# Kernel optimization log

Hardware: AMD Instinct MI355X
Metric: run time of the kernel (lower is better)

The kernel has to match this reference:

```python
import jax, jax.numpy as jnp
import numpy as np
import math

B, S, D = 4, 1024, 1024
H, DK = 16, 64
NUM_BUCKETS, MAX_DIST = 32, 128


def _relative_position_bucket(relative_position, num_buckets=NUM_BUCKETS, max_distance=MAX_DIST):
    # bidirectional bucketing (T5 encoder style)
    num_buckets = num_buckets // 2
    buckets = (relative_position > 0).astype(jnp.int32) * num_buckets
    rp = jnp.abs(relative_position)
    max_exact = num_buckets // 2
    is_small = rp < max_exact
    # clamp to >=1 to avoid log(0); masked out by is_small anyway
    rp_large = max_exact + (
        jnp.log(jnp.maximum(rp, 1).astype(jnp.float32) / max_exact)
        / math.log(max_distance / max_exact)
        * (num_buckets - max_exact)
    ).astype(jnp.int32)
    rp_large = jnp.minimum(rp_large, num_buckets - 1)
    return buckets + jnp.where(is_small, rp, rp_large)


def compute_bias(rel_bias_table, q_len, k_len):
    ctx = jnp.arange(q_len)[:, None]
    mem = jnp.arange(k_len)[None, :]
    buckets = _relative_position_bucket(mem - ctx)  # [q,k]
    values = rel_bias_table[buckets]  # [q,k,H]
    return jnp.transpose(values, (2, 0, 1))  # [H,q,k]


def setup_inputs() -> dict:
    key = jax.random.key(0)
    ks = jax.random.split(key, 6)
    return {
        "hidden_states": jax.random.normal(ks[0], (B, S, D), dtype=jnp.float32),
        "Wq": jax.random.normal(ks[1], (D, H * DK), dtype=jnp.float32) * 0.02,
        "Wk": jax.random.normal(ks[2], (D, H * DK), dtype=jnp.float32) * 0.02,
        "Wv": jax.random.normal(ks[3], (D, H * DK), dtype=jnp.float32) * 0.02,
        "Wo": jax.random.normal(ks[4], (H * DK, D), dtype=jnp.float32) * 0.02,
        "rel_bias_table": jax.random.normal(ks[5], (NUM_BUCKETS, H), dtype=jnp.float32),
    }


def reference(hidden_states, Wq, Wk, Wv, Wo, rel_bias_table):
    b, s, _ = hidden_states.shape
    # projections (no bias), split heads -> [b,h,s,dk]
    def heads(x):
        return jnp.transpose(x.reshape(b, s, H, DK), (0, 2, 1, 3))
    q = heads(hidden_states @ Wq)
    k = heads(hidden_states @ Wk)
    v = heads(hidden_states @ Wv)
    # NOTE: T5 attention is UNSCALED (no 1/sqrt(dk))
    scores = jnp.einsum("bhqd,bhkd->bhqk", q, k)
    bias = compute_bias(rel_bias_table, s, s)[None]  # [1,H,s,s]
    scores = scores + bias
    attn = jax.nn.softmax(scores.astype(jnp.float32), axis=-1).astype(scores.dtype)
    out = jnp.einsum("bhqk,bhkd->bhqd", attn, v)
    out = jnp.transpose(out, (0, 2, 1, 3)).reshape(b, s, H * DK)
    return out @ Wo
```

## Files before the change

### kernel.cpp

```cpp
#include <hip/hip_runtime.h>
#include <hip/hip_bf16.h>

typedef __attribute__((ext_vector_type(8))) short short8;
typedef __attribute__((ext_vector_type(4))) float f32x4;
typedef __attribute__((ext_vector_type(4))) unsigned u32x4;
typedef unsigned short u16;

#define AS1 __attribute__((address_space(1)))
#define AS3 __attribute__((address_space(3)))

#define LOG2E 1.44269504088896f
#define FOLD_M 46.166241308446828f
#define EXP2(x) __builtin_amdgcn_exp2f(x)
#define WAITV(n) asm volatile("s_waitcnt vmcnt(" #n ")" ::: "memory")
#define BAR() __builtin_amdgcn_s_barrier()

__device__ __forceinline__ u16 f2bf(float f) {
    unsigned u = __builtin_bit_cast(unsigned, f);
    u += 0x7FFFu + ((u >> 16) & 1u);
    return (u16)(u >> 16);
}

__device__ __forceinline__ unsigned pk2(float a, float b) {
    unsigned ua = __builtin_bit_cast(unsigned, a) + 0x8000u;
    unsigned ub = __builtin_bit_cast(unsigned, b) + 0x8000u;
    return __builtin_amdgcn_perm(ub, ua, 0x07060302);
}

__global__ __launch_bounds__(256) void k_prep(const float* __restrict__ hidden,
                                              const float* __restrict__ Wq, const float* __restrict__ Wk,
                                              const float* __restrict__ Wv, const float* __restrict__ Wo,
                                              const float* __restrict__ tbl,
                                              u16* __restrict__ hidb,
                                              u16* __restrict__ wt, u16* __restrict__ wot,
                                              float* __restrict__ bias2) {
    int z = blockIdx.z;
    if (z >= 5) {
        int i = ((z - 5) * 1024 + blockIdx.y * 32 + blockIdx.x) * 256 + threadIdx.x;
        float4 v = ((const float4*)hidden)[i];
        ushort4 o;
        o.x = f2bf(v.x); o.y = f2bf(v.y); o.z = f2bf(v.z); o.w = f2bf(v.w);
        ((ushort4*)hidb)[i] = o;
        return;
    }
    if (z == 4) {
        int idx = (blockIdx.y * 32 + blockIdx.x) * 256 + threadIdx.x;
        if (idx < 16 * 2048) {
            int r = idx & 2047, h = idx >> 11;
            int rel = r - 1023;
            int bucket = rel > 0 ? 16 : 0;
            int rp = rel < 0 ? -rel : rel;
            if (rp < 8) bucket += rp;
            else {
                int lb = 8 + (int)(log2f((float)rp * 0.125f) * 2.0f);
                bucket += (lb < 15 ? lb : 15);
            }
            bias2[idx] = tbl[bucket * 16 + h] * LOG2E - FOLD_M;
        }
        return;
    }
    const float* in = z == 0 ? Wq : z == 1 ? Wk : z == 2 ? Wv : Wo;
    u16* out = (z == 3) ? wot : wt + (size_t)z * 1024 * 1024;
    __shared__ float tile[32][33];
    int tx = threadIdx.x & 31, ty = threadIdx.x >> 5;
    int bx = blockIdx.x << 5, by = blockIdx.y << 5;
    #pragma unroll
    for (int j = 0; j < 32; j += 8)
        tile[ty + j][tx] = in[(size_t)(by + ty + j) * 1024 + bx + tx];
    __syncthreads();
    #pragma unroll
    for (int j = 0; j < 32; j += 8)
        out[(size_t)(bx + ty + j) * 1024 + by + tx] = f2bf(tile[tx][ty + j]);
}

__global__ __launch_bounds__(512, 2) void k_qkv(const u16* __restrict__ A, const u16* __restrict__ Bt,
                                                u16* __restrict__ oq, u16* __restrict__ ok,
                                                u16* __restrict__ ov) {
    __shared__ __align__(16) u16 As[2][256 * 64];
    __shared__ __align__(16) u16 Bs[2][192 * 64];
    int t = threadIdx.x, lane = t & 63, wave = t >> 6;
    int g = lane >> 4, ln = lane & 15;
    int wr = wave >> 2, wc = wave & 3;

    int bid = blockIdx.x;
    int xcd = bid & 7, wgl = bid >> 3;
    int mt = ((xcd & 3) << 2) + (wgl >> 3);
    int nt = ((xcd >> 2) << 3) + (wgl & 7);
    int m0 = mt << 8, n0 = nt * 192;

    f32x4 acc[8][3];
    #pragma unroll
    for (int i = 0; i < 8; i++)
        #pragma unroll
        for (int j = 0; j < 3; j++) acc[i][j] = (f32x4){0.f, 0.f, 0.f, 0.f};

    #define QSTG(kt_, buf_)                                                                      \
        {                                                                                        \
            _Pragma("unroll")                                                                    \
            for (int u = 0; u < 4; u++) {                                                        \
                int L = t * 16 + u * 8192;                                                       \
                int row = L >> 7, gI = (L >> 4) & 7, gp = gI ^ (row & 7);                        \
                __builtin_amdgcn_global_load_lds(                                                \
                    (const AS1 void*)(A + (size_t)(m0 + row) * 1024 + (kt_) * 64 + gp * 8),      \
                    (AS3 void*)&As[buf_][L >> 1], 16, 0, 0);                                     \
            }                                                                                    \
            _Pragma("unroll")                                                                    \
            for (int u = 0; u < 3; u++) {                                                        \
                int L = t * 16 + u * 8192;                                                       \
                int row = L >> 7, gI = (L >> 4) & 7, gp = gI ^ (row & 7);                        \
                __builtin_amdgcn_global_load_lds(                                                \
                    (const AS1 void*)(Bt + (size_t)(n0 + row) * 1024 + (kt_) * 64 + gp * 8),     \
                    (AS3 void*)&Bs[buf_][L >> 1], 16, 0, 0);                                     \
            }                                                                                    \
        }

    QSTG(0, 0);

    #pragma unroll 2
    for (int kt = 0; kt < 16; kt++) {
        const int c = kt & 1;
        if (kt < 15) {
            QSTG(kt + 1, c ^ 1);
            WAITV(7);
        } else {
            WAITV(0);
        }
        BAR();

        #pragma unroll
        for (int ks = 0; ks < 2; ks++) {
            short8 af[8], bfr[3];
            int cb = ((ks << 2) + g) << 4;
            #pragma unroll
            for (int mf = 0; mf < 8; mf++) {
                int row = (wr << 7) + (mf << 4) + ln;
                af[mf] = *(const short8*)((const char*)&As[c][0] + row * 128 + (cb ^ ((row & 7) << 4)));
            }
            #pragma unroll
            for (int nf = 0; nf < 3; nf++) {
                int row = wc * 48 + (nf << 4) + ln;
                bfr[nf] = *(const short8*)((const char*)&Bs[c][0] + row * 128 + (cb ^ ((row & 7) << 4)));
            }
            #pragma unroll
            for (int mf = 0; mf < 8; mf++)
                #pragma unroll
                for (int nf = 0; nf < 3; nf++)
                    acc[mf][nf] = __builtin_amdgcn_mfma_f32_16x16x32_bf16(af[mf], bfr[nf], acc[mf][nf], 0, 0, 0);
        }
        BAR();
    }
    #undef QSTG

    #pragma unroll
    for (int mf = 0; mf < 8; mf++)
        #pragma unroll
        for (int nf = 0; nf < 3; nf++) {
            int mb = m0 + (wr << 7) + (mf << 4) + (g << 2);
            int n = n0 + wc * 48 + (nf << 4) + ln;
            int j = n >> 10, col = n & 1023;
            int h = col >> 6, dk = col & 63;
            int b = mb >> 10, s = mb & 1023;
            if (j == 2) {
                ushort4 pk;
                pk.x = f2bf(acc[mf][nf][0]); pk.y = f2bf(acc[mf][nf][1]);
                pk.z = f2bf(acc[mf][nf][2]); pk.w = f2bf(acc[mf][nf][3]);
                *(ushort4*)(ov + ((size_t)(((b << 4) + h) * 64 + dk)) * 1024 + s) = pk;
            } else {
                u16* dst = (j == 0) ? oq : ok;
                #pragma unroll
                for (int r = 0; r < 4; r++)
                    dst[((size_t)(((b << 4) + h) * 1024 + s + r)) * 64 + dk] = f2bf(acc[mf][nf][r]);
            }
        }
}

__global__ __launch_bounds__(256) void k_gemm_out(const u16* __restrict__ A, const u16* __restrict__ Bt,
                                                  float* __restrict__ outf) {
    const int K = 1024, N = 1024;
    __shared__ __align__(16) u16 As[2][8192];
    __shared__ __align__(16) u16 Bs[2][8192];
    int t = threadIdx.x, lane = t & 63, wave = t >> 6;
    int bid = blockIdx.y * 8 + blockIdx.x;
    int sbid = (bid & 7) * 32 + (bid >> 3);
    int m0 = (sbid >> 3) << 7, n0 = (sbid & 7) << 7;
    int wm = (wave >> 1) << 6, wn = (wave & 1) << 6;
    int g = lane >> 4, ln = lane & 15;
    f32x4 acc[4][4];
    #pragma unroll
    for (int i = 0; i < 4; i++)
        #pragma unroll
        for (int j = 0; j < 4; j++) acc[i][j] = (f32x4){0.f, 0.f, 0.f, 0.f};

    int schunk = ((lane & 3) ^ ((lane >> 3) & 3)) << 3;
    const u16* gA = A + (size_t)(m0 + wave * 16 + (lane >> 2)) * K + schunk;
    const u16* gB = Bt + (size_t)(n0 + wave * 16 + (lane >> 2)) * K + schunk;
    int ldsOff = wave * 512;

    #define GSTAGE(k0_, buf_)                                                                          \
        {                                                                                              \
            __builtin_amdgcn_global_load_lds((const AS1 void*)(gA + (k0_)),                            \
                                             (AS3 void*)&As[buf_][ldsOff], 16, 0, 0);                  \
            __builtin_amdgcn_global_load_lds((const AS1 void*)(gA + 64 * K + (k0_)),                   \
                                             (AS3 void*)&As[buf_][ldsOff + 2048], 16, 0, 0);           \
            __builtin_amdgcn_global_load_lds((const AS1 void*)(gB + (k0_)),                            \
                                             (AS3 void*)&Bs[buf_][ldsOff], 16, 0, 0);                  \
            __builtin_amdgcn_global_load_lds((const AS1 void*)(gB + 64 * K + (k0_)),                   \
                                             (AS3 void*)&Bs[buf_][ldsOff + 2048], 16, 0, 0);           \
        }

    GSTAGE(0, 0);

    int rchunk = (g ^ ((ln >> 1) & 3)) << 3;

    #pragma unroll 2
    for (int kb = 0; kb < 32; kb++) {
        const int cur = kb & 1;
        if (kb < 31) {
            GSTAGE((kb + 1) * 32, cur ^ 1);
            WAITV(4);
        } else {
            WAITV(0);
        }
        BAR();

        short8 af[4], bfr[4];
        #pragma unroll
        for (int fm = 0; fm < 4; fm++)
            af[fm] = *(const short8*)&As[cur][(wm + (fm << 4) + ln) * 32 + rchunk];
        #pragma unroll
        for (int fn = 0; fn < 4; fn++)
            bfr[fn] = *(const short8*)&Bs[cur][(wn + (fn << 4) + ln) * 32 + rchunk];
        #pragma unroll
        for (int fm = 0; fm < 4; fm++)
            #pragma unroll
            for (int fn = 0; fn < 4; fn++)
                acc[fm][fn] = __builtin_amdgcn_mfma_f32_16x16x32_bf16(af[fm], bfr[fn], acc[fm][fn], 0, 0, 0);

        BAR();
    }

    #pragma unroll
    for (int fm = 0; fm < 4; fm++)
        #pragma unroll
        for (int fn = 0; fn < 4; fn++) {
            int mb = m0 + wm + (fm << 4) + (g << 2);
            int n = n0 + wn + (fn << 4) + ln;
            #pragma unroll
            for (int r = 0; r < 4; r++)
                outf[(size_t)(mb + r) * N + n] = acc[fm][fn][r];
        }
    #undef GSTAGE
}

__global__ __launch_bounds__(256, 2) void k_attn(const u16* __restrict__ Qg, const u16* __restrict__ Kg,
                                                 const u16* __restrict__ Vtg, const float* __restrict__ bias2,
                                                 u16* __restrict__ attn_out) {
    __shared__ __align__(16) u16 Ks[2][64 * 64];
    __shared__ __align__(16) u16 Vts[2][64 * 64];
    __shared__ __align__(16) float blds4[4][1160];

    int t = threadIdx.x, lane = t & 63, w = t >> 6;
    int bid = blockIdx.x;
    int sid = (bid & 7) * 64 + (bid >> 3);
    int qb = sid & 7, h = (sid >> 3) & 15, b = sid >> 7;
    int q0 = qb << 7;
    const u16* Qh = Qg + ((size_t)(((b << 4) + h) * 1024 + q0)) * 64;
    const u16* Kh = Kg + (size_t)(((b << 4) + h)) * 1024 * 64;
    const u16* Vth = Vtg + (size_t)(((b << 4) + h)) * 64 * 1024;
    const float* bh = bias2 + (h << 11);

    int g = lane >> 4, ln = lane & 15;
    int lnk = (ln & 3) | ((ln & 4) << 1) | ((ln & 8) >> 1);
    int kbq = ((g & 1) << 3) | ((g >> 1) << 2);

    short8 qf[2][2];
    #pragma unroll
    for (int fm = 0; fm < 2; fm++)
        #pragma unroll
        for (int kh = 0; kh < 2; kh++)
            qf[fm][kh] = *(const short8*)(Qh + (size_t)(w * 32 + fm * 16 + ln) * 64 + kh * 32 + g * 8);

    int w0 = 896 - q0;
    for (int i = t; i < 1152; i += 256) {
        float v = bh[w0 + i];
        #pragma unroll
        for (int a2 = 0; a2 < 4; a2++) { int x = i - a2; if (x >= 0) blds4[a2][x] = v; }
    }
    float b_hi = bh[1023 + 256];
    float b_lo = bh[1023 - 256];
    int aRep = (3 - ln) & 3;
    const float* repB = &blds4[aRep][0];

    #define STAGE(kb_, buf_)                                                                     \
        {                                                                                        \
            _Pragma("unroll")                                                                    \
            for (int r2 = 0; r2 < 2; r2++) {                                                     \
                int L = t * 16 + r2 * 4096;                                                      \
                int row = L >> 7, gI = (L >> 4) & 7, gp = gI ^ (row & 7);                        \
                __builtin_amdgcn_global_load_lds(                                                \
                    (const AS1 void*)(Kh + (size_t)((kb_) * 64 + row) * 64 + gp * 8),            \
                    (AS3 void*)&Ks[buf_][L >> 1], 16, 0, 0);                                     \
                __builtin_amdgcn_global_load_lds(                                                \
                    (const AS1 void*)(Vth + (size_t)row * 1024 + (kb_) * 64 + gp * 8),           \
                    (AS3 void*)&Vts[buf_][L >> 1], 16, 0, 0);                                    \
            }                                                                                    \
        }

    STAGE(0, 0);
    asm volatile("s_waitcnt lgkmcnt(0)" ::: "memory");
    __syncthreads();

    float psum[2] = {0.f, 0.f};
    f32x4 o[2][4];
    #pragma unroll
    for (int fm = 0; fm < 2; fm++)
        #pragma unroll
        for (int dn = 0; dn < 4; dn++) o[fm][dn] = (f32x4){0.f, 0.f, 0.f, 0.f};

    #pragma unroll 2
    for (int kb = 0; kb < 16; kb++) {
        const int cur = kb & 1;
        if (kb < 15) {
            STAGE(kb + 1, cur ^ 1);
            WAITV(4);
        } else {
            WAITV(0);
        }
        BAR();

        f32x4 s[2][4];
        __builtin_amdgcn_s_setprio(1);
        #pragma unroll
        for (int fn = 0; fn < 4; fn++) {
            int row = (fn << 4) + lnk;
            short8 kf0 = *(const short8*)((const char*)Ks[cur] + row * 128 + (((g << 4) + 0)  ^ ((row & 7) << 4)));
            short8 kf1 = *(const short8*)((const char*)Ks[cur] + row * 128 + (((g << 4) + 64) ^ ((row & 7) << 4)));
            #pragma unroll
            for (int fm = 0; fm < 2; fm++) {
                f32x4 a = (f32x4){0.f, 0.f, 0.f, 0.f};
                a = __builtin_amdgcn_mfma_f32_16x16x32_bf16(kf0, qf[fm][0], a, 0, 0, 0);
                a = __builtin_amdgcn_mfma_f32_16x16x32_bf16(kf1, qf[fm][1], a, 0, 0, 0);
                s[fm][fn] = a;
            }
        }
        __builtin_amdgcn_s_setprio(0);

        int d0 = 64 * kb - q0 - 32 * w;
        int ibase = 64 * kb - 32 * w + 127 + kbq - ln;
        bool fast = (d0 >= 122) || (d0 <= -154);
        float bu = d0 > 0 ? b_hi : b_lo;
        unsigned Px[2][4], Py[2][4];
        #pragma unroll
        for (int fm = 0; fm < 2; fm++)
            #pragma unroll
            for (int fn = 0; fn < 4; fn++) {
                f32x4 sv = s[fm][fn];
                float b0, b1, b2v, b3;
                if (fast) { b0 = b1 = b2v = b3 = bu; }
                else {
                    float4 bb = *(const float4*)(repB + (ibase + 16 * fn - 16 * fm - aRep));
                    b0 = bb.x; b1 = bb.y; b2v = bb.z; b3 = bb.w;
                }
                float p0 = EXP2(fmaf(sv[0], LOG2E, b0));
                float p1 = EXP2(fmaf(sv[1], LOG2E, b1));
                float p2 = EXP2(fmaf(sv[2], LOG2E, b2v));
                float p3 = EXP2(fmaf(sv[3], LOG2E, b3));
                psum[fm] += (p0 + p1) + (p2 + p3);
                Px[fm][fn] = pk2(p0, p1);
                Py[fm][fn] = pk2(p2, p3);
            }

        short8 pa[2][2];
        #pragma unroll
        for (int fm = 0; fm < 2; fm++)
            #pragma unroll
            for (int ks = 0; ks < 2; ks++) {
                unsigned w0r = Px[fm][2 * ks], w2r = Px[fm][2 * ks + 1];
                unsigned w1r = Py[fm][2 * ks], w3r = Py[fm][2 * ks + 1];
                asm volatile("s_nop 1\n\tv_permlane32_swap_b32 %0, %1" : "+v"(w0r), "+v"(w2r));
                asm volatile("s_nop 1\n\tv_permlane32_swap_b32 %0, %1" : "+v"(w1r), "+v"(w3r));
                u32x4 tv; tv[0] = w0r; tv[1] = w1r; tv[2] = w2r; tv[3] = w3r;
                pa[fm][ks] = __builtin_bit_cast(short8, tv);
            }

        __builtin_amdgcn_s_setprio(1);
        #pragma unroll
        for (int dn = 0; dn < 4; dn++) {
            int vrow = (dn << 4) + ln;
            short8 vb0 = *(const short8*)((const char*)Vts[cur] + vrow * 128 + (((g << 4) + 0)  ^ ((vrow & 7) << 4)));
            short8 vb1 = *(const short8*)((const char*)Vts[cur] + vrow * 128 + (((g << 4) + 64) ^ ((vrow & 7) << 4)));
            #pragma unroll
            for (int fm = 0; fm < 2; fm++) {
                f32x4 a = o[fm][dn];
                a = __builtin_amdgcn_mfma_f32_16x16x32_bf16(pa[fm][0], vb0, a, 0, 0, 0);
                a = __builtin_amdgcn_mfma_f32_16x16x32_bf16(pa[fm][1], vb1, a, 0, 0, 0);
                o[fm][dn] = a;
            }
        }
        __builtin_amdgcn_s_setprio(0);

        BAR();
    }

    float linv[2][4];
    #pragma unroll
    for (int fm = 0; fm < 2; fm++) {
        float v = psum[fm];
        v += __shfl_xor(v, 16);
        v += __shfl_xor(v, 32);
        float inv = 1.0f / v;
        #pragma unroll
        for (int r = 0; r < 4; r++)
            linv[fm][r] = __shfl(inv, 4 * g + r);
    }
    #pragma unroll
    for (int fm = 0; fm < 2; fm++)
        #pragma unroll
        for (int dn = 0; dn < 4; dn++)
            #pragma unroll
            for (int r = 0; r < 4; r++) {
                int srow = q0 + 32 * w + 16 * fm + (g << 2) + r;
                int col = (h << 6) + (dn << 4) + ln;
                attn_out[((size_t)((b << 10) + srow) << 10) + col] = f2bf(o[fm][dn][r] * linv[fm][r]);
            }
}

extern "C" void kernel_launch(void* const* d_in, const int* in_sizes, int n_in,
                              void* d_out, int out_size, void* d_ws, size_t ws_size,
                              hipStream_t stream) {
    const float* hidden = (const float*)d_in[0];
    const float* Wq = (const float*)d_in[1];
    const float* Wk = (const float*)d_in[2];
    const float* Wv = (const float*)d_in[3];
    const float* Wo = (const float*)d_in[4];
    const float* tbl = (const float*)d_in[5];

    u16* hidb = (u16*)d_ws;
    u16* wt   = hidb + 4096 * 1024;
    u16* wot  = wt + 3072 * 1024;
    u16* Qb   = wot + 1024 * 1024;
    u16* Kb   = Qb + 4 * 16 * 1024 * 64;
    u16* Vb   = Kb + 4 * 16 * 1024 * 64;
    u16* attn = Vb + 4 * 16 * 1024 * 64;
    float* bias = (float*)(attn + 4096 * 1024);

    k_prep<<<dim3(32, 32, 9), 256, 0, stream>>>(hidden, Wq, Wk, Wv, Wo, tbl, hidb, wt, wot, bias);
    k_qkv<<<256, 512, 0, stream>>>(hidb, wt, Qb, Kb, Vb);
    k_attn<<<512, 256, 0, stream>>>(Qb, Kb, Vb, bias, attn);
    k_gemm_out<<<dim3(8, 32), 256, 0, stream>>>(attn, wot, (float*)d_out);
}
```

Before: 93.99 us.

## Load K/V fragments directly from global memory, dropping LDS staging and barriers

The attention kernel stops staging K and V tiles into double-buffered shared memory with global_load_lds and barriers. Each wave now loads its MFMA fragments for K and V straight from global memory, relying on L1/L2 caching for reuse across the four waves. The launch bound rises to 3 blocks per CU since LDS use drops. Each wave now reads K and V redundantly, and there is no explicit prefetch, so load latency may be exposed.

```diff
diff --git a/kernel.cpp b/kernel.cpp
--- a/kernel.cpp
+++ b/kernel.cpp
@@ -252,11 +252,9 @@
     #undef GSTAGE
 }
 
-__global__ __launch_bounds__(256, 2) void k_attn(const u16* __restrict__ Qg, const u16* __restrict__ Kg,
+__global__ __launch_bounds__(256, 3) void k_attn(const u16* __restrict__ Qg, const u16* __restrict__ Kg,
                                                  const u16* __restrict__ Vtg, const float* __restrict__ bias2,
                                                  u16* __restrict__ attn_out) {
-    __shared__ __align__(16) u16 Ks[2][64 * 64];
-    __shared__ __align__(16) u16 Vts[2][64 * 64];
     __shared__ __align__(16) float blds4[4][1160];
 
     int t = threadIdx.x, lane = t & 63, w = t >> 6;
@@ -291,24 +289,10 @@
     int aRep = (3 - ln) & 3;
     const float* repB = &blds4[aRep][0];
 
-    #define STAGE(kb_, buf_)                                                                     \
-        {                                                                                        \
-            _Pragma("unroll")                                                                    \
-            for (int r2 = 0; r2 < 2; r2++) {                                                     \
-                int L = t * 16 + r2 * 4096;                                                      \
-                int row = L >> 7, gI = (L >> 4) & 7, gp = gI ^ (row & 7);                        \
-                __builtin_amdgcn_global_load_lds(                                                \
-                    (const AS1 void*)(Kh + (size_t)((kb_) * 64 + row) * 64 + gp * 8),            \
-                    (AS3 void*)&Ks[buf_][L >> 1], 16, 0, 0);                                     \
-                __builtin_amdgcn_global_load_lds(                                                \
-                    (const AS1 void*)(Vth + (size_t)row * 1024 + (kb_) * 64 + gp * 8),           \
-                    (AS3 void*)&Vts[buf_][L >> 1], 16, 0, 0);                                    \
-            }                                                                                    \
-        }
-
-    STAGE(0, 0);
-    asm volatile("s_waitcnt lgkmcnt(0)" ::: "memory");
     __syncthreads();
+
+    const u16* Kf = Kh + (size_t)lnk * 64 + g * 8;
+    const u16* Vf = Vth + (size_t)ln * 1024 + g * 8;
 
     float psum[2] = {0.f, 0.f};
     f32x4 o[2][4];
@@ -319,22 +303,13 @@
 
     #pragma unroll 2
     for (int kb = 0; kb < 16; kb++) {
-        const int cur = kb & 1;
-        if (kb < 15) {
-            STAGE(kb + 1, cur ^ 1);
-            WAITV(4);
-        } else {
-            WAITV(0);
-        }
-        BAR();
-
         f32x4 s[2][4];
         __builtin_amdgcn_s_setprio(1);
         #pragma unroll
         for (int fn = 0; fn < 4; fn++) {
-            int row = (fn << 4) + lnk;
-            short8 kf0 = *(const short8*)((const char*)Ks[cur] + row * 128 + (((g << 4) + 0)  ^ ((row & 7) << 4)));
-            short8 kf1 = *(const short8*)((const char*)Ks[cur] + row * 128 + (((g << 4) + 64) ^ ((row & 7) << 4)));
+            const u16* kr = Kf + (size_t)kb * 4096 + fn * 1024;
+            short8 kf0 = *(const short8*)(kr);
+            short8 kf1 = *(const short8*)(kr + 32);
             #pragma unroll
             for (int fm = 0; fm < 2; fm++) {
                 f32x4 a = (f32x4){0.f, 0.f, 0.f, 0.f};
@@ -344,6 +319,14 @@
             }
         }
         __builtin_amdgcn_s_setprio(0);
+
+        short8 vb[4][2];
+        #pragma unroll
+        for (int dn = 0; dn < 4; dn++) {
+            const u16* vr = Vf + dn * 16384 + kb * 64;
+            vb[dn][0] = *(const short8*)(vr);
+            vb[dn][1] = *(const short8*)(vr + 32);
+        }
 
         int d0 = 64 * kb - q0 - 32 * w;
         int ibase = 64 * kb - 32 * w + 127 + kbq - ln;
@@ -385,21 +368,15 @@
 
         __builtin_amdgcn_s_setprio(1);
         #pragma unroll
-        for (int dn = 0; dn < 4; dn++) {
-            int vrow = (dn << 4) + ln;
-            short8 vb0 = *(const short8*)((const char*)Vts[cur] + vrow * 128 + (((g << 4) + 0)  ^ ((vrow & 7) << 4)));
-            short8 vb1 = *(const short8*)((const char*)Vts[cur] + vrow * 128 + (((g << 4) + 64) ^ ((vrow & 7) << 4)));
+        for (int dn = 0; dn < 4; dn++)
             #pragma unroll
             for (int fm = 0; fm < 2; fm++) {
                 f32x4 a = o[fm][dn];
-                a = __builtin_amdgcn_mfma_f32_16x16x32_bf16(pa[fm][0], vb0, a, 0, 0, 0);
-                a = __builtin_amdgcn_mfma_f32_16x16x32_bf16(pa[fm][1], vb1, a, 0, 0, 0);
+                a = __builtin_amdgcn_mfma_f32_16x16x32_bf16(pa[fm][0], vb[dn][0], a, 0, 0, 0);
+                a = __builtin_amdgcn_mfma_f32_16x16x32_bf16(pa[fm][1], vb[dn][1], a, 0, 0, 0);
                 o[fm][dn] = a;
             }
-        }
         __builtin_amdgcn_s_setprio(0);
-
-        BAR();
     }
 
     float linv[2][4];
```

After: 164.8 us. +75.4%, slower.

## Retile QKV GEMM to 128x128 tiles with 256-thread blocks and BK=32

Applied to the files above, without the earlier changes.

Replaces the 256x192-tile, 512-thread QKV projection GEMM with 128x128 tiles, 4 waves per block, and a K-step of 32 with a smaller LDS footprint. This mirrors the output GEMM's structure. The change raises the block count from 256 to 768 and allows more resident blocks per CU, aiming for better occupancy and load balance across CUs. In exchange each tile reuses its operands less, so global/L2 traffic rises, and twice as many K iterations mean more barriers.

```diff
diff --git a/kernel.cpp b/kernel.cpp
--- a/kernel.cpp
+++ b/kernel.cpp
@@ -73,103 +73,92 @@
         out[(size_t)(bx + ty + j) * 1024 + by + tx] = f2bf(tile[tx][ty + j]);
 }
 
-__global__ __launch_bounds__(512, 2) void k_qkv(const u16* __restrict__ A, const u16* __restrict__ Bt,
+__global__ __launch_bounds__(256, 4) void k_qkv(const u16* __restrict__ A, const u16* __restrict__ Bt,
                                                 u16* __restrict__ oq, u16* __restrict__ ok,
                                                 u16* __restrict__ ov) {
-    __shared__ __align__(16) u16 As[2][256 * 64];
-    __shared__ __align__(16) u16 Bs[2][192 * 64];
+    const int K = 1024;
+    __shared__ __align__(16) u16 As[2][4096];
+    __shared__ __align__(16) u16 Bs[2][4096];
     int t = threadIdx.x, lane = t & 63, wave = t >> 6;
+    int bid = blockIdx.y * 24 + blockIdx.x;
+    int sbid = (bid & 7) * 96 + (bid >> 3);
+    int m0 = (sbid / 24) << 7, n0 = (sbid % 24) << 7;
+    int wm = (wave >> 1) << 6, wn = (wave & 1) << 6;
     int g = lane >> 4, ln = lane & 15;
-    int wr = wave >> 2, wc = wave & 3;
-
-    int bid = blockIdx.x;
-    int xcd = bid & 7, wgl = bid >> 3;
-    int mt = ((xcd & 3) << 2) + (wgl >> 3);
-    int nt = ((xcd >> 2) << 3) + (wgl & 7);
-    int m0 = mt << 8, n0 = nt * 192;
-
-    f32x4 acc[8][3];
-    #pragma unroll
-    for (int i = 0; i < 8; i++)
-        #pragma unroll
-        for (int j = 0; j < 3; j++) acc[i][j] = (f32x4){0.f, 0.f, 0.f, 0.f};
-
-    #define QSTG(kt_, buf_)                                                                      \
-        {                                                                                        \
-            _Pragma("unroll")                                                                    \
-            for (int u = 0; u < 4; u++) {                                                        \
-                int L = t * 16 + u * 8192;                                                       \
-                int row = L >> 7, gI = (L >> 4) & 7, gp = gI ^ (row & 7);                        \
-                __builtin_amdgcn_global_load_lds(                                                \
-                    (const AS1 void*)(A + (size_t)(m0 + row) * 1024 + (kt_) * 64 + gp * 8),      \
-                    (AS3 void*)&As[buf_][L >> 1], 16, 0, 0);                                     \
-            }                                                                                    \
-            _Pragma("unroll")                                                                    \
-            for (int u = 0; u < 3; u++) {                                                        \
-                int L = t * 16 + u * 8192;                                                       \
-                int row = L >> 7, gI = (L >> 4) & 7, gp = gI ^ (row & 7);                        \
-                __builtin_amdgcn_global_load_lds(                                                \
-                    (const AS1 void*)(Bt + (size_t)(n0 + row) * 1024 + (kt_) * 64 + gp * 8),     \
-                    (AS3 void*)&Bs[buf_][L >> 1], 16, 0, 0);                                     \
-            }                                                                                    \
+    f32x4 acc[4][4];
+    #pragma unroll
+    for (int i = 0; i < 4; i++)
+        #pragma unroll
+        for (int j = 0; j < 4; j++) acc[i][j] = (f32x4){0.f, 0.f, 0.f, 0.f};
+
+    int schunk = ((lane & 3) ^ ((lane >> 3) & 3)) << 3;
+    const u16* gA = A + (size_t)(m0 + wave * 16 + (lane >> 2)) * K + schunk;
+    const u16* gB = Bt + (size_t)(n0 + wave * 16 + (lane >> 2)) * K + schunk;
+    int ldsOff = wave * 512;
+
+    #define QSTG(k0_, buf_)                                                                            \
+        {                                                                                              \
+            __builtin_amdgcn_global_load_lds((const AS1 void*)(gA + (k0_)),                            \
+                                             (AS3 void*)&As[buf_][ldsOff], 16, 0, 0);                  \
+            __builtin_amdgcn_global_load_lds((const AS1 void*)(gA + 64 * K + (k0_)),                   \
+                                             (AS3 void*)&As[buf_][ldsOff + 2048], 16, 0, 0);           \
+            __builtin_amdgcn_global_load_lds((const AS1 void*)(gB + (k0_)),                            \
+                                             (AS3 void*)&Bs[buf_][ldsOff], 16, 0, 0);                  \
+            __builtin_amdgcn_global_load_lds((const AS1 void*)(gB + 64 * K + (k0_)),                   \
+                                             (AS3 void*)&Bs[buf_][ldsOff + 2048], 16, 0, 0);           \
         }
 
     QSTG(0, 0);
 
+    int rchunk = (g ^ ((ln >> 1) & 3)) << 3;
+
     #pragma unroll 2
-    for (int kt = 0; kt < 16; kt++) {
-        const int c = kt & 1;
-        if (kt < 15) {
-            QSTG(kt + 1, c ^ 1);
-            WAITV(7);
+    for (int kb = 0; kb < 32; kb++) {
+        const int cur = kb & 1;
+        if (kb < 31) {
+            QSTG((kb + 1) * 32, cur ^ 1);
+            WAITV(4);
         } else {
             WAITV(0);
         }
         BAR();
 
-        #pragma unroll
-        for (int ks = 0; ks < 2; ks++) {
-            short8 af[8], bfr[3];
-            int cb = ((ks << 2) + g) << 4;
-            #pragma unroll
-            for (int mf = 0; mf < 8; mf++) {
-                int row = (wr << 7) + (mf << 4) + ln;
-                af[mf] = *(const short8*)((const char*)&As[c][0] + row * 128 + (cb ^ ((row & 7) << 4)));
-            }
-            #pragma unroll
-            for (int nf = 0; nf < 3; nf++) {
-                int row = wc * 48 + (nf << 4) + ln;
-                bfr[nf] = *(const short8*)((const char*)&Bs[c][0] + row * 128 + (cb ^ ((row & 7) << 4)));
-            }
-            #pragma unroll
-            for (int mf = 0; mf < 8; mf++)
-                #pragma unroll
-                for (int nf = 0; nf < 3; nf++)
-                    acc[mf][nf] = __builtin_amdgcn_mfma_f32_16x16x32_bf16(af[mf], bfr[nf], acc[mf][nf], 0, 0, 0);
-        }
+        short8 af[4], bfr[4];
+        #pragma unroll
+        for (int fm = 0; fm < 4; fm++)
+            af[fm] = *(const short8*)&As[cur][(wm + (fm << 4) + ln) * 32 + rchunk];
+        #pragma unroll
+        for (int fn = 0; fn < 4; fn++)
+            bfr[fn] = *(const short8*)&Bs[cur][(wn + (fn << 4) + ln) * 32 + rchunk];
+        #pragma unroll
+        for (int fm = 0; fm < 4; fm++)
+            #pragma unroll
+            for (int fn = 0; fn < 4; fn++)
+                acc[fm][fn] = __builtin_amdgcn_mfma_f32_16x16x32_bf16(af[fm], bfr[fn], acc[fm][fn], 0, 0, 0);
+
         BAR();
     }
     #undef QSTG
 
     #pragma unroll
-    for (int mf = 0; mf < 8; mf++)
-        #pragma unroll
-        for (int nf = 0; nf < 3; nf++) {
-            int mb = m0 + (wr << 7) + (mf << 4) + (g << 2);
-            int n = n0 + wc * 48 + (nf << 4) + ln;
+    for (int fm = 0; fm < 4; fm++)
+        #pragma unroll
+        for (int fn = 0; fn < 4; fn++) {
+            int mb = m0 + wm + (fm << 4) + (g << 2);
+            int n = n0 + wn + (fn << 4) + ln;
             int j = n >> 10, col = n & 1023;
             int h = col >> 6, dk = col & 63;
             int b = mb >> 10, s = mb & 1023;
             if (j == 2) {
                 ushort4 pk;
-                pk.x = f2bf(acc[mf][nf][0]); pk.y = f2bf(acc[mf][nf][1]);
-                pk.z = f2bf(acc[mf][nf][2]); pk.w = f2bf(acc[mf][nf][3]);
+                pk.x = f2bf(acc[fm][fn][0]); pk.y = f2bf(acc[fm][fn][1]);
+                pk.z = f2bf(acc[fm][fn][2]); pk.w = f2bf(acc[fm][fn][3]);
                 *(ushort4*)(ov + ((size_t)(((b << 4) + h) * 64 + dk)) * 1024 + s) = pk;
             } else {
                 u16* dst = (j == 0) ? oq : ok;
                 #pragma unroll
                 for (int r = 0; r < 4; r++)
-                    dst[((size_t)(((b << 4) + h) * 1024 + s + r)) * 64 + dk] = f2bf(acc[mf][nf][r]);
+                    dst[((size_t)(((b << 4) + h) * 1024 + s + r)) * 64 + dk] = f2bf(acc[fm][fn][r]);
             }
         }
 }
@@ -445,7 +434,7 @@
     float* bias = (float*)(attn + 4096 * 1024);
 
     k_prep<<<dim3(32, 32, 9), 256, 0, stream>>>(hidden, Wq, Wk, Wv, Wo, tbl, hidb, wt, wot, bias);
-    k_qkv<<<256, 512, 0, stream>>>(hidb, wt, Qb, Kb, Vb);
+    k_qkv<<<dim3(24, 32), 256, 0, stream>>>(hidb, wt, Qb, Kb, Vb);
     k_attn<<<512, 256, 0, stream>>>(Qb, Kb, Vb, bias, attn);
     k_gemm_out<<<dim3(8, 32), 256, 0, stream>>>(attn, wot, (float*)d_out);
 }
```

New measurement: 96.86 us. 3.0% more time.
